# Performance work log

Hardware: AMD Instinct MI355X
Metric: run time of the kernel (lower is better)

The kernel has to match this reference:

```python
import jax, jax.numpy as jnp
import numpy as np

B, H, S, D = 2, 16, 2048, 64

def setup_inputs() -> dict:
    key = jax.random.key(0)
    kq, kk, kv = jax.random.split(key, 3)
    Q = jax.random.normal(kq, (B, H, S, D), dtype=jnp.float32)
    K = jax.random.normal(kk, (B, H, S, D), dtype=jnp.float32)
    V = jax.random.normal(kv, (B, H, S, D), dtype=jnp.float32)
    # causal mask, broadcastable over batch/heads: True = attend
    mask = jnp.tril(jnp.ones((S, S), dtype=bool))[None, None, :, :]
    return {"Q": Q, "K": K, "V": V, "mask": mask}

def reference(Q, K, V, mask):
    d_k = Q.shape[-1]
    scale = 1.0 / jnp.sqrt(jnp.asarray(d_k, Q.dtype))
    # [..., q, k] scores; mask applied as -inf before softmax (matches torch.where)
    scores = jnp.einsum('bhqd,bhkd->bhqk', Q, K) * scale
    scores = jnp.where(mask, scores, -jnp.inf)
    weights = jax.nn.softmax(scores, axis=-1)
    out = jnp.einsum('bhqk,bhkd->bhqd', weights, V)
    return out
```

## Files before the change

kernel.cpp:

```cpp
#include <hip/hip_runtime.h>
#include <hip/hip_bf16.h>

#define S_LEN 2048
#define D_DIM 64
#define NBH   32
#define NE    (NBH * S_LEN * D_DIM)

typedef __attribute__((ext_vector_type(8))) short bf16x8;
typedef __attribute__((ext_vector_type(4))) short s16x4;
typedef __attribute__((ext_vector_type(2))) unsigned u32x2;
typedef __attribute__((ext_vector_type(4))) float f32x4;
typedef __attribute__((ext_vector_type(4))) unsigned short us4;

__device__ __forceinline__ unsigned short bf16rne(float x) {
  unsigned u = __builtin_bit_cast(unsigned, x);
  u += 0x7fffu + ((u >> 16) & 1u);
  return (unsigned short)(u >> 16);
}
__device__ __forceinline__ float bf16tof(unsigned short h) {
  return __builtin_bit_cast(float, (unsigned)h << 16);
}
__device__ __forceinline__ void bf16split(float x, unsigned short& h, unsigned short& l) {
  h = bf16rne(x);
  float r = x - bf16tof(h);
  l = bf16rne(r);
}

__device__ __forceinline__ f32x4 mfma16(bf16x8 a, bf16x8 b, f32x4 c) {
  return __builtin_amdgcn_mfma_f32_16x16x32_bf16(a, b, c, 0, 0, 0);
}

__device__ __forceinline__ void gload16(const void* g, void* l) {
  __builtin_amdgcn_global_load_lds(
      (const __attribute__((address_space(1))) unsigned*)g,
      (__attribute__((address_space(3))) unsigned*)l, 16, 0, 0);
}

__device__ __forceinline__ unsigned cvtpk(float a, float b) {
  unsigned r;
  asm("v_cvt_pk_bf16_f32 %0, %1, %2" : "=v"(r) : "v"(a), "v"(b));
  return r;
}

__global__ __launch_bounds__(256) void prepass(const float* __restrict__ K,
                                               const float* __restrict__ V,
                                               unsigned short* __restrict__ Kh,
                                               unsigned short* __restrict__ Kl,
                                               unsigned short* __restrict__ Vh,
                                               unsigned short* __restrict__ Vl) {
  __shared__ float t[64][65];
  const int tid = threadIdx.x;
  if (blockIdx.x < 4096) {
    const int i = ((int)blockIdx.x * 256 + tid) * 4;
    float4 v = *(const float4*)(K + i);
    float a[4] = {v.x, v.y, v.z, v.w};
    us4 h, l;
#pragma unroll
    for (int j = 0; j < 4; ++j) {
      unsigned short hh, ll;
      bf16split(a[j], hh, ll);
      h[j] = hh; l[j] = ll;
    }
    *(us4*)(Kh + i) = h;
    *(us4*)(Kl + i) = l;
  } else {
    const int bid = (int)blockIdx.x - 4096;
    const int bh  = bid >> 5;
    const int kv0 = (bid & 31) << 6;
#pragma unroll
    for (int pp = 0; pp < 4; ++pp) {
      const int r  = (tid >> 4) + pp * 16;
      const int c4 = (tid & 15) << 2;
      float4 v = *(const float4*)(V + ((size_t)bh * S_LEN + kv0 + r) * D_DIM + c4);
      t[r][c4] = v.x; t[r][c4 + 1] = v.y; t[r][c4 + 2] = v.z; t[r][c4 + 3] = v.w;
    }
    __syncthreads();
    const int d  = tid >> 2;
    const int k0 = (tid & 3) << 4;
    bf16x8 h0, h1, l0, l1;
#pragma unroll
    for (int j = 0; j < 8; ++j) {
      unsigned short hh, ll;
      bf16split(t[k0 + j][d], hh, ll);
      h0[j] = (short)hh; l0[j] = (short)ll;
    }
#pragma unroll
    for (int j = 0; j < 8; ++j) {
      unsigned short hh, ll;
      bf16split(t[k0 + 8 + j][d], hh, ll);
      h1[j] = (short)hh; l1[j] = (short)ll;
    }
    const size_t ob = ((size_t)bh * D_DIM + d) * S_LEN + kv0 + k0;
    *(bf16x8*)(Vh + ob)     = h0;
    *(bf16x8*)(Vh + ob + 8) = h1;
    *(bf16x8*)(Vl + ob)     = l0;
    *(bf16x8*)(Vl + ob + 8) = l1;
  }
}

__global__ __launch_bounds__(256) void attn_main(const float* __restrict__ Q,
                                                 const unsigned short* __restrict__ Kh,
                                                 const unsigned short* __restrict__ Kl,
                                                 const unsigned short* __restrict__ Vh,
                                                 const unsigned short* __restrict__ Vl,
                                                 float* __restrict__ Out) {
  __shared__ __align__(16) char smem[24576];
  unsigned short* sKh = (unsigned short*)smem;
  unsigned short* sKl = (unsigned short*)(smem + 4096);
  unsigned short* sVh = (unsigned short*)(smem + 8192);
  unsigned short* sVl = (unsigned short*)(smem + 12288);
  short*          sPh = (short*)(smem + 16384);
  short*          sPl = (short*)(smem + 20480);

  const int tid   = threadIdx.x;
  const int bh    = blockIdx.x & 31;
  const int qt    = 31 - (blockIdx.x >> 5);
  const int qbase = qt << 6;
  const int wave  = tid >> 6;
  const int lane  = tid & 63;
  const int c     = lane & 15;
  const int g     = lane >> 4;
  const int qw    = qbase + (wave << 4);

  const size_t bhO = (size_t)bh * (S_LEN * D_DIM);

  const float SC = 0.125f * 1.44269504088896340736f;
  bf16x8 qh[2], ql[2];
#pragma unroll
  for (int ch = 0; ch < 2; ++ch) {
    const float* src = Q + bhO + (size_t)(qw + c) * D_DIM + ch * 32 + g * 8;
    float4 v0 = *(const float4*)src;
    float4 v1 = *(const float4*)(src + 4);
    float a[8] = {v0.x, v0.y, v0.z, v0.w, v1.x, v1.y, v1.z, v1.w};
#pragma unroll
    for (int e = 0; e < 8; ++e) {
      unsigned short hh, ll;
      bf16split(a[e] * SC, hh, ll);
      qh[ch][e] = (short)hh;
      ql[ch][e] = (short)ll;
    }
  }

  f32x4 acc[4] = {{0.f,0.f,0.f,0.f},{0.f,0.f,0.f,0.f},{0.f,0.f,0.f,0.f},{0.f,0.f,0.f,0.f}};
  float m_r = -3.0e38f, l_r = 0.f;

  const unsigned short* gKh = Kh + bhO;
  const unsigned short* gKl = Kl + bhO;
  const unsigned short* gVh = Vh + bhO;
  const unsigned short* gVl = Vl + bhO;

  const int rs   = tid >> 3;
  const int kswz = ((tid & 7) ^ (rs & 7)) << 3;
  const int vrow = tid >> 2;
  const int vcol = (((tid & 3) ^ (vrow & 3)) << 3);

  unsigned short* dK_h = sKh + (wave << 9);
  unsigned short* dK_l = sKl + (wave << 9);
  unsigned short* dV_h = sVh + (wave << 9);
  unsigned short* dV_l = sVl + (wave << 9);

  const int nIter = (qbase >> 5) + 2;
  for (int it = 0; it < nIter; ++it) {
    const int kv0 = it << 5;
    gload16(gKh + (size_t)(kv0 + rs) * D_DIM + kswz, dK_h);
    gload16(gKl + (size_t)(kv0 + rs) * D_DIM + kswz, dK_l);
    gload16(gVh + (size_t)vrow * S_LEN + kv0 + vcol, dV_h);
    gload16(gVl + (size_t)vrow * S_LEN + kv0 + vcol, dV_l);
    __syncthreads();

    if (kv0 <= qw + 15) {
      f32x4 sj[2];
#pragma unroll
      for (int j = 0; j < 2; ++j) {
        const int row = (j << 4) + c;
        bf16x8 kfh[2], kfl[2];
#pragma unroll
        for (int ch = 0; ch < 2; ++ch) {
          const int p = ((ch << 2) + g) ^ (c & 7);
          kfh[ch] = *(const bf16x8*)&sKh[(row << 6) + (p << 3)];
          kfl[ch] = *(const bf16x8*)&sKl[(row << 6) + (p << 3)];
        }
        f32x4 sa = {0.f, 0.f, 0.f, 0.f};
        sa = mfma16(kfh[0], qh[0], sa);
        sa = mfma16(kfh[1], qh[1], sa);
        sa = mfma16(kfh[0], ql[0], sa);
        sa = mfma16(kfh[1], ql[1], sa);
        sa = mfma16(kfl[0], qh[0], sa);
        sa = mfma16(kfl[1], qh[1], sa);
        sj[j] = sa;
      }
      if (kv0 + 31 > qw) {
#pragma unroll
        for (int j = 0; j < 2; ++j) {
          const int kvb = kv0 + (j << 4) + (g << 2);
#pragma unroll
          for (int r = 0; r < 4; ++r) {
            if (kvb + r > qw + c) sj[j][r] = -3.0e38f;
          }
        }
      }
      float pm = fmaxf(fmaxf(fmaxf(sj[0][0], sj[0][1]), fmaxf(sj[0][2], sj[0][3])),
                       fmaxf(fmaxf(sj[1][0], sj[1][1]), fmaxf(sj[1][2], sj[1][3])));
      pm = fmaxf(pm, __shfl_xor(pm, 16));
      pm = fmaxf(pm, __shfl_xor(pm, 32));
      const float mn  = fmaxf(m_r, pm);
      const float fac = exp2f(m_r - mn);
      m_r = mn;
      float p[2][4];
      float ps = 0.f;
#pragma unroll
      for (int j = 0; j < 2; ++j)
#pragma unroll
        for (int r = 0; r < 4; ++r) {
          p[j][r] = exp2f(sj[j][r] - mn);
          ps += p[j][r];
        }
      ps += __shfl_xor(ps, 16);
      ps += __shfl_xor(ps, 32);
      l_r = l_r * fac + ps;
#pragma unroll
      for (int dt = 0; dt < 4; ++dt)
#pragma unroll
        for (int r = 0; r < 4; ++r) acc[dt][r] *= fac;

#pragma unroll
      for (int j = 0; j < 2; ++j) {
        const unsigned H0 = cvtpk(p[j][0], p[j][1]);
        const unsigned H1 = cvtpk(p[j][2], p[j][3]);
        const float f0 = __builtin_bit_cast(float, H0 << 16);
        const float f1 = __builtin_bit_cast(float, H0 & 0xffff0000u);
        const float f2 = __builtin_bit_cast(float, H1 << 16);
        const float f3 = __builtin_bit_cast(float, H1 & 0xffff0000u);
        const unsigned L0 = cvtpk(p[j][0] - f0, p[j][1] - f1);
        const unsigned L1 = cvtpk(p[j][2] - f2, p[j][3] - f3);
        const int blkp = ((j << 1) + (g >> 1)) ^ (c & 3);
        const int dw   = (wave << 8) + (c << 4) + (blkp << 2) + ((g & 1) << 1);
        u32x2 hw; hw[0] = H0; hw[1] = H1;
        u32x2 lw; lw[0] = L0; lw[1] = L1;
        *(s16x4*)&sPh[dw << 1] = __builtin_bit_cast(s16x4, hw);
        *(s16x4*)&sPl[dw << 1] = __builtin_bit_cast(s16x4, lw);
      }
      const int rdw = (wave << 8) + (c << 4) + ((g ^ (c & 3)) << 2);
      const bf16x8 pbh = *(const bf16x8*)&sPh[rdw << 1];
      const bf16x8 pbl = *(const bf16x8*)&sPl[rdw << 1];

#pragma unroll
      for (int dt = 0; dt < 4; ++dt) {
        const int vb = (((dt << 4) + c) << 5) + ((g ^ (c & 3)) << 3);
        const bf16x8 vfh = *(const bf16x8*)&sVh[vb];
        const bf16x8 vfl = *(const bf16x8*)&sVl[vb];
        acc[dt] = mfma16(vfh, pbh, acc[dt]);
        acc[dt] = mfma16(vfl, pbh, acc[dt]);
        acc[dt] = mfma16(vfh, pbl, acc[dt]);
      }
    }
    __syncthreads();
  }

  const float inv = 1.0f / l_r;
  float (*ob)[68] = (float(*)[68])smem;
#pragma unroll
  for (int dt = 0; dt < 4; ++dt)
#pragma unroll
    for (int r = 0; r < 4; ++r)
      ob[(wave << 4) + c][(dt << 4) + (g << 2) + r] = acc[dt][r] * inv;
  __syncthreads();
#pragma unroll
  for (int v = 0; v < 4; ++v) {
    const int row = (tid >> 4) + (v << 4);
    const int dc  = (tid & 15) << 2;
    float4 val = *(const float4*)&ob[row][dc];
    *(float4*)(Out + bhO + (size_t)(qbase + row) * D_DIM + dc) = val;
  }
}

extern "C" void kernel_launch(void* const* d_in, const int* in_sizes, int n_in,
                              void* d_out, int out_size, void* d_ws, size_t ws_size,
                              hipStream_t stream) {
  const float* Q = (const float*)d_in[0];
  const float* K = (const float*)d_in[1];
  const float* V = (const float*)d_in[2];

  unsigned short* Kh = (unsigned short*)d_ws;
  unsigned short* Kl = Kh + NE;
  unsigned short* Vh = Kl + NE;
  unsigned short* Vl = Vh + NE;
  float* Out = (float*)d_out;

  prepass<<<5120, 256, 0, stream>>>(K, V, Kh, Kl, Vh, Vl);
  attn_main<<<NBH * (S_LEN / 64), 256, 0, stream>>>(Q, Kh, Kl, Vh, Vl, Out);
}
```

Baseline: 200.6 us.

## Double-buffer K/V tiles, skip redundant rescales, use hardware bf16 split conversions

K/V tiles are now double-buffered in LDS: the next tile's global-to-LDS loads are issued before the current tile is computed, which leaves one barrier per iteration instead of two. The online-softmax rescale of acc and l is skipped when no row max increases. The manual bf16 hi/lo split is replaced with packed v_cvt_pk_bf16_f32 conversions, and the K prepass handles 8 elements per thread with fewer blocks. The LDS swizzle for P/V reads and the output store are also changed. LDS use grows from 24KB to 40KB per block, which may lower occupancy.

```diff
diff --git a/kernel.cpp b/kernel.cpp
--- a/kernel.cpp
+++ b/kernel.cpp
@@ -9,22 +9,8 @@
 typedef __attribute__((ext_vector_type(8))) short bf16x8;
 typedef __attribute__((ext_vector_type(4))) short s16x4;
 typedef __attribute__((ext_vector_type(2))) unsigned u32x2;
+typedef __attribute__((ext_vector_type(4))) unsigned u32x4;
 typedef __attribute__((ext_vector_type(4))) float f32x4;
-typedef __attribute__((ext_vector_type(4))) unsigned short us4;
-
-__device__ __forceinline__ unsigned short bf16rne(float x) {
-  unsigned u = __builtin_bit_cast(unsigned, x);
-  u += 0x7fffu + ((u >> 16) & 1u);
-  return (unsigned short)(u >> 16);
-}
-__device__ __forceinline__ float bf16tof(unsigned short h) {
-  return __builtin_bit_cast(float, (unsigned)h << 16);
-}
-__device__ __forceinline__ void bf16split(float x, unsigned short& h, unsigned short& l) {
-  h = bf16rne(x);
-  float r = x - bf16tof(h);
-  l = bf16rne(r);
-}
 
 __device__ __forceinline__ f32x4 mfma16(bf16x8 a, bf16x8 b, f32x4 c) {
   return __builtin_amdgcn_mfma_f32_16x16x32_bf16(a, b, c, 0, 0, 0);
@@ -39,6 +25,14 @@
 __device__ __forceinline__ unsigned cvtpk(float a, float b) {
   unsigned r;
   asm("v_cvt_pk_bf16_f32 %0, %1, %2" : "=v"(r) : "v"(a), "v"(b));
+  return r;
+}
+__device__ __forceinline__ u32x2 split2(float a, float b) {
+  u32x2 r;
+  r.x = cvtpk(a, b);
+  const float fa = __builtin_bit_cast(float, r.x << 16);
+  const float fb = __builtin_bit_cast(float, r.x & 0xffff0000u);
+  r.y = cvtpk(a - fa, b - fb);
   return r;
 }
 
@@ -50,21 +44,20 @@
                                                unsigned short* __restrict__ Vl) {
   __shared__ float t[64][65];
   const int tid = threadIdx.x;
-  if (blockIdx.x < 4096) {
-    const int i = ((int)blockIdx.x * 256 + tid) * 4;
-    float4 v = *(const float4*)(K + i);
-    float a[4] = {v.x, v.y, v.z, v.w};
-    us4 h, l;
-#pragma unroll
-    for (int j = 0; j < 4; ++j) {
-      unsigned short hh, ll;
-      bf16split(a[j], hh, ll);
-      h[j] = hh; l[j] = ll;
-    }
-    *(us4*)(Kh + i) = h;
-    *(us4*)(Kl + i) = l;
+  if (blockIdx.x < 2048) {
+    const int i = ((int)blockIdx.x * 256 + tid) * 8;
+    float4 v0 = *(const float4*)(K + i);
+    float4 v1 = *(const float4*)(K + i + 4);
+    u32x4 H, L;
+    u32x2 s;
+    s = split2(v0.x, v0.y); H[0] = s.x; L[0] = s.y;
+    s = split2(v0.z, v0.w); H[1] = s.x; L[1] = s.y;
+    s = split2(v1.x, v1.y); H[2] = s.x; L[2] = s.y;
+    s = split2(v1.z, v1.w); H[3] = s.x; L[3] = s.y;
+    *(u32x4*)(Kh + i) = H;
+    *(u32x4*)(Kl + i) = L;
   } else {
-    const int bid = (int)blockIdx.x - 4096;
+    const int bid = (int)blockIdx.x - 2048;
     const int bh  = bid >> 5;
     const int kv0 = (bid & 31) << 6;
 #pragma unroll
@@ -77,24 +70,22 @@
     __syncthreads();
     const int d  = tid >> 2;
     const int k0 = (tid & 3) << 4;
-    bf16x8 h0, h1, l0, l1;
-#pragma unroll
-    for (int j = 0; j < 8; ++j) {
-      unsigned short hh, ll;
-      bf16split(t[k0 + j][d], hh, ll);
-      h0[j] = (short)hh; l0[j] = (short)ll;
-    }
-#pragma unroll
-    for (int j = 0; j < 8; ++j) {
-      unsigned short hh, ll;
-      bf16split(t[k0 + 8 + j][d], hh, ll);
-      h1[j] = (short)hh; l1[j] = (short)ll;
+    u32x4 H0, L0, H1, L1;
+#pragma unroll
+    for (int jj = 0; jj < 4; ++jj) {
+      u32x2 s = split2(t[k0 + 2 * jj][d], t[k0 + 2 * jj + 1][d]);
+      H0[jj] = s.x; L0[jj] = s.y;
+    }
+#pragma unroll
+    for (int jj = 0; jj < 4; ++jj) {
+      u32x2 s = split2(t[k0 + 8 + 2 * jj][d], t[k0 + 9 + 2 * jj][d]);
+      H1[jj] = s.x; L1[jj] = s.y;
     }
     const size_t ob = ((size_t)bh * D_DIM + d) * S_LEN + kv0 + k0;
-    *(bf16x8*)(Vh + ob)     = h0;
-    *(bf16x8*)(Vh + ob + 8) = h1;
-    *(bf16x8*)(Vl + ob)     = l0;
-    *(bf16x8*)(Vl + ob + 8) = l1;
+    *(u32x4*)(Vh + ob)     = H0;
+    *(u32x4*)(Vh + ob + 8) = H1;
+    *(u32x4*)(Vl + ob)     = L0;
+    *(u32x4*)(Vl + ob + 8) = L1;
   }
 }
 
@@ -104,13 +95,13 @@
                                                  const unsigned short* __restrict__ Vh,
                                                  const unsigned short* __restrict__ Vl,
                                                  float* __restrict__ Out) {
-  __shared__ __align__(16) char smem[24576];
+  __shared__ __align__(16) char smem[40960];
   unsigned short* sKh = (unsigned short*)smem;
-  unsigned short* sKl = (unsigned short*)(smem + 4096);
-  unsigned short* sVh = (unsigned short*)(smem + 8192);
-  unsigned short* sVl = (unsigned short*)(smem + 12288);
-  short*          sPh = (short*)(smem + 16384);
-  short*          sPl = (short*)(smem + 20480);
+  unsigned short* sKl = (unsigned short*)(smem + 8192);
+  unsigned short* sVh = (unsigned short*)(smem + 16384);
+  unsigned short* sVl = (unsigned short*)(smem + 24576);
+  short*          sPh = (short*)(smem + 32768);
+  short*          sPl = (short*)(smem + 36864);
 
   const int tid   = threadIdx.x;
   const int bh    = blockIdx.x & 31;
@@ -132,13 +123,14 @@
     float4 v0 = *(const float4*)src;
     float4 v1 = *(const float4*)(src + 4);
     float a[8] = {v0.x, v0.y, v0.z, v0.w, v1.x, v1.y, v1.z, v1.w};
-#pragma unroll
-    for (int e = 0; e < 8; ++e) {
-      unsigned short hh, ll;
-      bf16split(a[e] * SC, hh, ll);
-      qh[ch][e] = (short)hh;
-      ql[ch][e] = (short)ll;
-    }
+    u32x4 H, L;
+    u32x2 s;
+    s = split2(a[0] * SC, a[1] * SC); H[0] = s.x; L[0] = s.y;
+    s = split2(a[2] * SC, a[3] * SC); H[1] = s.x; L[1] = s.y;
+    s = split2(a[4] * SC, a[5] * SC); H[2] = s.x; L[2] = s.y;
+    s = split2(a[6] * SC, a[7] * SC); H[3] = s.x; L[3] = s.y;
+    qh[ch] = __builtin_bit_cast(bf16x8, H);
+    ql[ch] = __builtin_bit_cast(bf16x8, L);
   }
 
   f32x4 acc[4] = {{0.f,0.f,0.f,0.f},{0.f,0.f,0.f,0.f},{0.f,0.f,0.f,0.f},{0.f,0.f,0.f,0.f}};
@@ -152,23 +144,33 @@
   const int rs   = tid >> 3;
   const int kswz = ((tid & 7) ^ (rs & 7)) << 3;
   const int vrow = tid >> 2;
-  const int vcol = (((tid & 3) ^ (vrow & 3)) << 3);
-
-  unsigned short* dK_h = sKh + (wave << 9);
-  unsigned short* dK_l = sKl + (wave << 9);
-  unsigned short* dV_h = sVh + (wave << 9);
-  unsigned short* dV_l = sVl + (wave << 9);
+  const int vcol = (((tid & 3) ^ ((tid >> 3) & 3)) << 3);
 
   const int nIter = (qbase >> 5) + 2;
+
+#define STAGE(itx, buf)                                                        \
+  do {                                                                         \
+    const int kv_ = (itx) << 5;                                                \
+    gload16(gKh + (size_t)(kv_ + rs) * D_DIM + kswz,                           \
+            sKh + ((buf) << 11) + (wave << 9));                                \
+    gload16(gKl + (size_t)(kv_ + rs) * D_DIM + kswz,                           \
+            sKl + ((buf) << 11) + (wave << 9));                                \
+    gload16(gVh + (size_t)vrow * S_LEN + kv_ + vcol,                           \
+            sVh + ((buf) << 11) + (wave << 9));                                \
+    gload16(gVl + (size_t)vrow * S_LEN + kv_ + vcol,                           \
+            sVl + ((buf) << 11) + (wave << 9));                                \
+  } while (0)
+
+  STAGE(0, 0);
+  __syncthreads();
+  int cur = 0;
+
   for (int it = 0; it < nIter; ++it) {
+    if (it + 1 < nIter) STAGE(it + 1, cur ^ 1);
     const int kv0 = it << 5;
-    gload16(gKh + (size_t)(kv0 + rs) * D_DIM + kswz, dK_h);
-    gload16(gKl + (size_t)(kv0 + rs) * D_DIM + kswz, dK_l);
-    gload16(gVh + (size_t)vrow * S_LEN + kv0 + vcol, dV_h);
-    gload16(gVl + (size_t)vrow * S_LEN + kv0 + vcol, dV_l);
-    __syncthreads();
 
     if (kv0 <= qw + 15) {
+      const int cb = cur << 11;
       f32x4 sj[2];
 #pragma unroll
       for (int j = 0; j < 2; ++j) {
@@ -177,8 +179,8 @@
 #pragma unroll
         for (int ch = 0; ch < 2; ++ch) {
           const int p = ((ch << 2) + g) ^ (c & 7);
-          kfh[ch] = *(const bf16x8*)&sKh[(row << 6) + (p << 3)];
-          kfl[ch] = *(const bf16x8*)&sKl[(row << 6) + (p << 3)];
+          kfh[ch] = *(const bf16x8*)&sKh[cb + (row << 6) + (p << 3)];
+          kfl[ch] = *(const bf16x8*)&sKl[cb + (row << 6) + (p << 3)];
         }
         f32x4 sa = {0.f, 0.f, 0.f, 0.f};
         sa = mfma16(kfh[0], qh[0], sa);
@@ -203,50 +205,45 @@
                        fmaxf(fmaxf(sj[1][0], sj[1][1]), fmaxf(sj[1][2], sj[1][3])));
       pm = fmaxf(pm, __shfl_xor(pm, 16));
       pm = fmaxf(pm, __shfl_xor(pm, 32));
-      const float mn  = fmaxf(m_r, pm);
-      const float fac = exp2f(m_r - mn);
-      m_r = mn;
+      if (!__all(pm <= m_r)) {
+        const float mn  = fmaxf(m_r, pm);
+        const float fac = exp2f(m_r - mn);
+        m_r = mn;
+        l_r *= fac;
+#pragma unroll
+        for (int dt = 0; dt < 4; ++dt) acc[dt] *= fac;
+      }
       float p[2][4];
       float ps = 0.f;
 #pragma unroll
       for (int j = 0; j < 2; ++j)
 #pragma unroll
         for (int r = 0; r < 4; ++r) {
-          p[j][r] = exp2f(sj[j][r] - mn);
+          p[j][r] = exp2f(sj[j][r] - m_r);
           ps += p[j][r];
         }
       ps += __shfl_xor(ps, 16);
       ps += __shfl_xor(ps, 32);
-      l_r = l_r * fac + ps;
-#pragma unroll
-      for (int dt = 0; dt < 4; ++dt)
-#pragma unroll
-        for (int r = 0; r < 4; ++r) acc[dt][r] *= fac;
+      l_r += ps;
 
 #pragma unroll
       for (int j = 0; j < 2; ++j) {
-        const unsigned H0 = cvtpk(p[j][0], p[j][1]);
-        const unsigned H1 = cvtpk(p[j][2], p[j][3]);
-        const float f0 = __builtin_bit_cast(float, H0 << 16);
-        const float f1 = __builtin_bit_cast(float, H0 & 0xffff0000u);
-        const float f2 = __builtin_bit_cast(float, H1 << 16);
-        const float f3 = __builtin_bit_cast(float, H1 & 0xffff0000u);
-        const unsigned L0 = cvtpk(p[j][0] - f0, p[j][1] - f1);
-        const unsigned L1 = cvtpk(p[j][2] - f2, p[j][3] - f3);
-        const int blkp = ((j << 1) + (g >> 1)) ^ (c & 3);
+        u32x2 s0 = split2(p[j][0], p[j][1]);
+        u32x2 s1 = split2(p[j][2], p[j][3]);
+        const int blkp = ((j << 1) + (g >> 1)) ^ ((c >> 1) & 3);
         const int dw   = (wave << 8) + (c << 4) + (blkp << 2) + ((g & 1) << 1);
-        u32x2 hw; hw[0] = H0; hw[1] = H1;
-        u32x2 lw; lw[0] = L0; lw[1] = L1;
+        u32x2 hw; hw[0] = s0.x; hw[1] = s1.x;
+        u32x2 lw; lw[0] = s0.y; lw[1] = s1.y;
         *(s16x4*)&sPh[dw << 1] = __builtin_bit_cast(s16x4, hw);
         *(s16x4*)&sPl[dw << 1] = __builtin_bit_cast(s16x4, lw);
       }
-      const int rdw = (wave << 8) + (c << 4) + ((g ^ (c & 3)) << 2);
+      const int rdw = (wave << 8) + (c << 4) + ((g ^ ((c >> 1) & 3)) << 2);
       const bf16x8 pbh = *(const bf16x8*)&sPh[rdw << 1];
       const bf16x8 pbl = *(const bf16x8*)&sPl[rdw << 1];
 
 #pragma unroll
       for (int dt = 0; dt < 4; ++dt) {
-        const int vb = (((dt << 4) + c) << 5) + ((g ^ (c & 3)) << 3);
+        const int vb = cb + (((dt << 4) + c) << 5) + ((g ^ ((c >> 1) & 3)) << 3);
         const bf16x8 vfh = *(const bf16x8*)&sVh[vb];
         const bf16x8 vfl = *(const bf16x8*)&sVl[vb];
         acc[dt] = mfma16(vfh, pbh, acc[dt]);
@@ -255,15 +252,16 @@
       }
     }
     __syncthreads();
+    cur ^= 1;
   }
 
   const float inv = 1.0f / l_r;
   float (*ob)[68] = (float(*)[68])smem;
 #pragma unroll
-  for (int dt = 0; dt < 4; ++dt)
-#pragma unroll
-    for (int r = 0; r < 4; ++r)
-      ob[(wave << 4) + c][(dt << 4) + (g << 2) + r] = acc[dt][r] * inv;
+  for (int dt = 0; dt < 4; ++dt) {
+    f32x4 o = acc[dt] * inv;
+    *(f32x4*)&ob[(wave << 4) + c][(dt << 4) + (g << 2)] = o;
+  }
   __syncthreads();
 #pragma unroll
   for (int v = 0; v < 4; ++v) {
@@ -287,6 +285,6 @@
   unsigned short* Vl = Vh + NE;
   float* Out = (float*)d_out;
 
-  prepass<<<5120, 256, 0, stream>>>(K, V, Kh, Kl, Vh, Vl);
+  prepass<<<3072, 256, 0, stream>>>(K, V, Kh, Kl, Vh, Vl);
   attn_main<<<NBH * (S_LEN / 64), 256, 0, stream>>>(Q, Kh, Kl, Vh, Vl, Out);
 }
```

Result: faster. 188.7 us (-5.9%).
